# Optimization experiments

Hardware: AMD Instinct MI355X
Metric: run time of the kernel (lower is better)

Reference implementation:

```python
import jax, jax.numpy as jnp
import numpy as np

B, S, D = 4, 4096, 1024
GROUP = 256
HEAD = 128
INNER = 2048


def setup_inputs() -> dict:
    key = jax.random.key(0)
    ks = jax.random.split(key, 16)
    s = 0.02
    return {
        'x': jax.random.normal(ks[0], (B, S, D), jnp.float32),
        'Wv': jax.random.normal(ks[1], (D, INNER), jnp.float32) * s,
        'bv': jnp.zeros((INNER,), jnp.float32),
        'Wg': jax.random.normal(ks[2], (D, INNER), jnp.float32) * s,
        'bg': jnp.zeros((INNER,), jnp.float32),
        'Win': jax.random.normal(ks[3], (D, HEAD), jnp.float32) * s,
        'bin_': jnp.zeros((HEAD,), jnp.float32),
        'Wout': jax.random.normal(ks[4], (INNER, D), jnp.float32) * s,
        'bout': jnp.zeros((D,), jnp.float32),
        'g_qq': 1.0 + jax.random.normal(ks[5], (HEAD,), jnp.float32) * s,
        'b_qq': jnp.zeros((HEAD,), jnp.float32),
        'g_qk': 1.0 + jax.random.normal(ks[6], (HEAD,), jnp.float32) * s,
        'b_qk': jnp.zeros((HEAD,), jnp.float32),
        'g_lq': 1.0 + jax.random.normal(ks[7], (HEAD,), jnp.float32) * s,
        'b_lq': jnp.zeros((HEAD,), jnp.float32),
        'g_lk': 1.0 + jax.random.normal(ks[8], (HEAD,), jnp.float32) * s,
        'b_lk': jnp.zeros((HEAD,), jnp.float32),
    }


def reference(x, Wv, bv, Wg, bg, Win, bin_, Wout, bout,
              g_qq, b_qq, g_qk, b_qk, g_lq, b_lq, g_lk, b_lk):
    b, s, d = x.shape
    g = s // GROUP
    xc = x.reshape(b, g, GROUP, d)                       # [B,G,C,D]
    v = jax.nn.silu(xc @ Wv + bv)                        # [B,G,C,E]
    gate = jax.nn.silu(xc @ Wg + bg)                     # [B,G,C,E]
    x_ = jax.nn.silu(xc @ Win + bin_)                    # [B,G,C,H]
    quad_q = x_ * g_qq + b_qq
    quad_k = x_ * g_qk + b_qk
    lin_q = x_ * g_lq + b_lq
    lin_k = x_ * g_lk + b_lk
    # local quadratic relu^2 attention per chunk
    scale = jnp.asarray(INNER ** 0.5, x.dtype)           # v.size(-1)**0.5
    attn = jnp.einsum('bgns,bgms->bgnm', quad_q, quad_k) / scale
    causal_mask = jnp.triu(jnp.ones((GROUP, GROUP), bool), 1)
    attn = jnp.where(causal_mask, 0.0, attn)
    attn = jnp.square(jax.nn.relu(attn))
    v_quad = jnp.einsum('bgnm,bgme->bgne', attn, v)
    # global causal linear attention: exclusive cumsum of per-chunk k^T v over chunks
    kv = jnp.einsum('bgcs,bgce->bgse', lin_k, v)         # [B,G,H,E]
    kv = jnp.cumsum(kv, axis=1) - kv                     # exclusive over chunk dim
    v_lin = jnp.einsum('bgcs,bgse->bgce', lin_q, kv)
    o = (v_quad + v_lin) * gate
    o = o @ Wout + bout
    return o.reshape(b, s, d)
```

## Files before the change

### kernel.cpp

```cpp
#include <hip/hip_runtime.h>

typedef __attribute__((ext_vector_type(8))) short short8;
typedef __attribute__((ext_vector_type(4))) float floatx4;
typedef __attribute__((ext_vector_type(4))) unsigned short ushort4v;
typedef unsigned short u16;

#define DEV __device__ __forceinline__

DEV u16 f2bf(float f) {
  unsigned int u = __float_as_uint(f);
  u += 0x7fffu + ((u >> 16) & 1u);
  return (u16)(u >> 16);
}
DEV float bf2f(u16 h) { return __uint_as_float(((unsigned int)h) << 16); }
DEV float silu_f(float x) { return x / (1.f + __expf(-x)); }
DEV floatx4 fzero() { floatx4 z = {0.f, 0.f, 0.f, 0.f}; return z; }
DEV floatx4 mfma16(short8 a, short8 b, floatx4 c) {
  return __builtin_amdgcn_mfma_f32_16x16x32_bf16(a, b, c, 0, 0, 0);
}
DEV void gll16(const void* g, void* l) {
  __builtin_amdgcn_global_load_lds((__attribute__((address_space(1))) void*)g,
                                   (__attribute__((address_space(3))) void*)l,
                                   16, 0, 0);
}

__global__ __launch_bounds__(256) void cast_x_kernel(const float* __restrict__ x,
                                                     u16* __restrict__ xb, int n4) {
  int i = blockIdx.x * 256 + threadIdx.x;
  if (i >= n4) return;
  float4 v = ((const float4*)x)[i];
  ushort4v o;
  o[0] = f2bf(v.x); o[1] = f2bf(v.y); o[2] = f2bf(v.z); o[3] = f2bf(v.w);
  *(ushort4v*)&xb[(size_t)i * 4] = o;
}

__global__ __launch_bounds__(256) void transpose_cast_kernel(const float* __restrict__ W,
                                                             u16* __restrict__ WT,
                                                             int K, int N) {
  __shared__ u16 tile[32][36];
  int n0 = blockIdx.x * 32, k0 = blockIdx.y * 32;
  int t = threadIdx.x;
  int r = t >> 3, cs = (t & 7) * 4;
  float4 v = *(const float4*)&W[(size_t)(k0 + r) * N + n0 + cs];
  tile[r][cs + 0] = f2bf(v.x);
  tile[r][cs + 1] = f2bf(v.y);
  tile[r][cs + 2] = f2bf(v.z);
  tile[r][cs + 3] = f2bf(v.w);
  __syncthreads();
  ushort4v o;
  o[0] = tile[cs + 0][r];
  o[1] = tile[cs + 1][r];
  o[2] = tile[cs + 2][r];
  o[3] = tile[cs + 3][r];
  *(ushort4v*)&WT[(size_t)(n0 + r) * K + k0 + cs] = o;
}

DEV void wave_transposed_store(u16* __restrict__ Ct, long chunk_stride,
                               const u16* trw, int chunk, int cbase, int nbase,
                               int lane) {
#pragma unroll
  for (int it = 0; it < 8; ++it) {
    int e_l = it * 8 + (lane >> 3);
    int c_off = (lane & 7) * 8;
    short8 val = *(const short8*)&trw[e_l * 72 + c_off];
    *(short8*)&Ct[(size_t)chunk * chunk_stride + (size_t)(nbase + e_l) * 256 + cbase +
                  c_off] = val;
  }
}

__global__ __launch_bounds__(256, 2) void gemm_vg(
    const u16* __restrict__ A, const u16* __restrict__ Bv, const u16* __restrict__ Bg,
    const float* __restrict__ bvb, const float* __restrict__ bgb,
    u16* __restrict__ vT, u16* __restrict__ gate) {
  constexpr int K = 1024, N = 2048;
  __shared__ union {
    struct { u16 a[128 * 64]; u16 b[2][128 * 64]; } st;
    u16 tr[4 * 64 * 72];
  } sm;
  const int t = threadIdx.x;
  const int wave = t >> 6, lane = t & 63;
  const int l15 = lane & 15, l16 = lane >> 4;
  const int ell = blockIdx.x;
  const int xcd = ell & 7, i = ell >> 3;
  const int m0 = (xcd * 16 + (i >> 4)) * 128;
  const int n0 = (i & 15) * 128;
  const int wm = (wave >> 1) * 64, wn = (wave & 1) * 64;

  floatx4 accv[4][4], accg[4][4];
#pragma unroll
  for (int a = 0; a < 4; ++a)
#pragma unroll
    for (int b = 0; b < 4; ++b) { accv[a][b] = fzero(); accg[a][b] = fzero(); }

  const u16 *pa[4], *pbv[4], *pbg[4];
#pragma unroll
  for (int j = 0; j < 4; ++j) {
    const int c = t + 256 * j;
    const int r = c >> 3, p = c & 7;
    const int g = p ^ (r & 7);
    const size_t off = (size_t)r * K + g * 8;
    pa[j] = A + (size_t)m0 * K + off;
    pbv[j] = Bv + (size_t)n0 * K + off;
    pbg[j] = Bg + (size_t)n0 * K + off;
  }

  for (int k0 = 0; k0 < K; k0 += 64) {
    __syncthreads();
#pragma unroll
    for (int j = 0; j < 4; ++j) {
      const int d = (t + 256 * j) * 8;
      gll16(pa[j] + k0, &sm.st.a[d]);
      gll16(pbv[j] + k0, &sm.st.b[0][d]);
      gll16(pbg[j] + k0, &sm.st.b[1][d]);
    }
    __syncthreads();
#pragma unroll
    for (int s = 0; s < 2; ++s) {
      short8 af[4], b0[4], b1[4];
#pragma unroll
      for (int mi = 0; mi < 4; ++mi) {
        const int wr = wm + mi * 16 + l15;
        af[mi] = *(const short8*)&sm.st.a[wr * 64 + ((s * 4 + l16) ^ (wr & 7)) * 8];
      }
#pragma unroll
      for (int ni = 0; ni < 4; ++ni) {
        const int wr = wn + ni * 16 + l15;
        const int sl = wr * 64 + ((s * 4 + l16) ^ (wr & 7)) * 8;
        b0[ni] = *(const short8*)&sm.st.b[0][sl];
        b1[ni] = *(const short8*)&sm.st.b[1][sl];
      }
#pragma unroll
      for (int mi = 0; mi < 4; ++mi)
#pragma unroll
        for (int ni = 0; ni < 4; ++ni) {
          accv[mi][ni] = mfma16(af[mi], b0[ni], accv[mi][ni]);
          accg[mi][ni] = mfma16(af[mi], b1[ni], accg[mi][ni]);
        }
    }
  }
  __syncthreads();

  u16* trw = &sm.tr[wave * 64 * 72];
#pragma unroll
  for (int mi = 0; mi < 4; ++mi)
#pragma unroll
    for (int ni = 0; ni < 4; ++ni) {
      const float bc = bvb[n0 + wn + ni * 16 + l15];
      ushort4v p;
#pragma unroll
      for (int r = 0; r < 4; ++r) p[r] = f2bf(silu_f(accv[mi][ni][r] + bc));
      *(ushort4v*)&trw[(ni * 16 + l15) * 72 + mi * 16 + l16 * 4] = p;
    }
  wave_transposed_store(vT, 2048L * 256, trw, (m0 + wm) >> 8, (m0 + wm) & 255,
                        n0 + wn, lane);
#pragma unroll
  for (int mi = 0; mi < 4; ++mi)
#pragma unroll
    for (int ni = 0; ni < 4; ++ni) {
      const float bc = bgb[n0 + wn + ni * 16 + l15];
#pragma unroll
      for (int r = 0; r < 4; ++r)
        trw[(mi * 16 + l16 * 4 + r) * 72 + ni * 16 + l15] =
            f2bf(silu_f(accg[mi][ni][r] + bc));
    }
#pragma unroll
  for (int it = 0; it < 8; ++it) {
    const int m_l = it * 8 + (lane >> 3);
    const int n_off = (lane & 7) * 8;
    *(short8*)&gate[(size_t)(m0 + wm + m_l) * N + n0 + wn + n_off] =
        *(const short8*)&trw[m_l * 72 + n_off];
  }
}

template <int MODE>
__global__ __launch_bounds__(256) void gemm_bt(
    const u16* __restrict__ A, const u16* __restrict__ Bt, int M, int N, int K,
    int nshift, const float* __restrict__ bias, u16* __restrict__ Cn,
    float* __restrict__ Cf, u16* __restrict__ Ct, long ct_stride,
    u16* __restrict__ Cn2, u16* __restrict__ Cn3,
    const float* __restrict__ gqq, const float* __restrict__ bqq,
    const float* __restrict__ gqk, const float* __restrict__ bqk,
    const float* __restrict__ glq, const float* __restrict__ blq,
    const float* __restrict__ glk, const float* __restrict__ blk) {
  __shared__ union {
    struct { u16 a[128 * 64]; u16 b[128 * 64]; } st;
    u16 tr[4 * 64 * 72];
  } sm;
  const int t = threadIdx.x;
  const int wave = t >> 6, lane = t & 63;
  const int l15 = lane & 15, l16 = lane >> 4;
  const int ell = blockIdx.x;
  const int xcd = ell & 7, i = ell >> 3;
  const int mtiles_per_xcd = M >> 10;
  const int m0 = (xcd * mtiles_per_xcd + (i >> nshift)) * 128;
  const int n0 = (i & ((1 << nshift) - 1)) * 128;
  const int wm = (wave >> 1) * 64, wn = (wave & 1) * 64;

  floatx4 acc[4][4];
#pragma unroll
  for (int i2 = 0; i2 < 4; ++i2)
#pragma unroll
    for (int j = 0; j < 4; ++j) acc[i2][j] = fzero();

  const u16* pa[4];
  const u16* pb[4];
#pragma unroll
  for (int j = 0; j < 4; ++j) {
    const int c = t + 256 * j;
    const int r = c >> 3, p = c & 7;
    const int g = p ^ (r & 7);
    pa[j] = A + (size_t)(m0 + r) * K + g * 8;
    pb[j] = Bt + (size_t)(n0 + r) * K + g * 8;
  }

  for (int k0 = 0; k0 < K; k0 += 64) {
    __syncthreads();
#pragma unroll
    for (int j = 0; j < 4; ++j) {
      gll16(pa[j] + k0, &sm.st.a[(t + 256 * j) * 8]);
      gll16(pb[j] + k0, &sm.st.b[(t + 256 * j) * 8]);
    }
    __syncthreads();
#pragma unroll
    for (int s = 0; s < 2; ++s) {
      short8 af[4], bfr[4];
#pragma unroll
      for (int mi = 0; mi < 4; ++mi) {
        const int wr = wm + mi * 16 + l15;
        af[mi] = *(const short8*)&sm.st.a[wr * 64 + ((s * 4 + l16) ^ (wr & 7)) * 8];
      }
#pragma unroll
      for (int ni = 0; ni < 4; ++ni) {
        const int wr = wn + ni * 16 + l15;
        bfr[ni] = *(const short8*)&sm.st.b[wr * 64 + ((s * 4 + l16) ^ (wr & 7)) * 8];
      }
#pragma unroll
      for (int mi = 0; mi < 4; ++mi)
#pragma unroll
        for (int ni = 0; ni < 4; ++ni)
          acc[mi][ni] = mfma16(af[mi], bfr[ni], acc[mi][ni]);
    }
  }
  __syncthreads();

  if constexpr (MODE == 3) {
#pragma unroll
    for (int mi = 0; mi < 4; ++mi)
#pragma unroll
      for (int ni = 0; ni < 4; ++ni) {
        const int col = n0 + wn + ni * 16 + l15;
        const float bc = bias[col];
        const int row = m0 + wm + mi * 16 + l16 * 4;
#pragma unroll
        for (int r = 0; r < 4; ++r)
          Cf[(size_t)(row + r) * N + col] = acc[mi][ni][r] + bc;
      }
  } else {
    u16* trw = &sm.tr[wave * 64 * 72];
#pragma unroll
    for (int mi = 0; mi < 4; ++mi)
#pragma unroll
      for (int ni = 0; ni < 4; ++ni) {
        const int col = wn + ni * 16 + l15;
        const float bc = bias[col];
        const float Gqq = gqq[col], Bqq = bqq[col];
        const float Gqk = gqk[col], Bqk = bqk[col];
        const float Glq = glq[col], Blq = blq[col];
        const float Glk = glk[col], Blk = blk[col];
        const int row = m0 + wm + mi * 16 + l16 * 4;
        ushort4v p;
#pragma unroll
        for (int r = 0; r < 4; ++r) {
          const float sv = silu_f(acc[mi][ni][r] + bc);
          const size_t ad = (size_t)(row + r) * N + col;
          Cn[ad] = f2bf(sv * Gqq + Bqq);
          Cn2[ad] = f2bf(sv * Gqk + Bqk);
          Cn3[ad] = f2bf(sv * Glq + Blq);
          p[r] = f2bf(sv * Glk + Blk);
        }
        *(ushort4v*)&trw[(ni * 16 + l15) * 72 + mi * 16 + l16 * 4] = p;
      }
    wave_transposed_store(Ct, ct_stride, trw, (m0 + wm) >> 8, (m0 + wm) & 255, wn,
                          lane);
  }
}

__global__ __launch_bounds__(256) void kv_kernel(const u16* __restrict__ vT,
                                                 const u16* __restrict__ lkT,
                                                 u16* __restrict__ kv) {
  const int chunk = blockIdx.y;
  const int et = blockIdx.x;
  const int w = threadIdx.x >> 6, lane = threadIdx.x & 63;
  const int l15 = lane & 15, l16 = lane >> 4;
  const size_t vb = (size_t)chunk * (2048 * 256) + (size_t)et * (128 * 256);
  const size_t lb = (size_t)chunk * (128 * 256);
  const int we = (w >> 1) * 64, wh = (w & 1) * 64;
  floatx4 acc[4][4];
#pragma unroll
  for (int i = 0; i < 4; ++i)
#pragma unroll
    for (int j = 0; j < 4; ++j) acc[i][j] = fzero();
  for (int kk = 0; kk < 8; ++kk) {
    short8 av[4], bv[4];
#pragma unroll
    for (int mi = 0; mi < 4; ++mi)
      av[mi] = *(const short8*)&vT[vb + (size_t)(we + mi * 16 + l15) * 256 + kk * 32 +
                                   l16 * 8];
#pragma unroll
    for (int ni = 0; ni < 4; ++ni)
      bv[ni] = *(const short8*)&lkT[lb + (size_t)(wh + ni * 16 + l15) * 256 + kk * 32 +
                                    l16 * 8];
#pragma unroll
    for (int mi = 0; mi < 4; ++mi)
#pragma unroll
      for (int ni = 0; ni < 4; ++ni) acc[mi][ni] = mfma16(av[mi], bv[ni], acc[mi][ni]);
  }
  u16* out = kv + (size_t)chunk * (2048 * 128);
#pragma unroll
  for (int mi = 0; mi < 4; ++mi)
#pragma unroll
    for (int ni = 0; ni < 4; ++ni) {
      const int h = wh + ni * 16 + l15;
      const int e = et * 128 + we + mi * 16 + l16 * 4;
#pragma unroll
      for (int r = 0; r < 4; ++r) out[(size_t)(e + r) * 128 + h] = f2bf(acc[mi][ni][r]);
    }
}

__global__ __launch_bounds__(256) void cumsum_kernel(u16* __restrict__ kv) {
  const int idx = blockIdx.x * 256 + threadIdx.x;
  const int b = blockIdx.y;
  float s = 0.f;
  for (int g = 0; g < 16; ++g) {
    const size_t a = (size_t)(b * 16 + g) * 262144 + idx;
    const float v = bf2f(kv[a]);
    kv[a] = f2bf(s);
    s += v;
  }
}

__global__ __launch_bounds__(256) void attn_kernel(
    const u16* __restrict__ qq, const u16* __restrict__ qk, const u16* __restrict__ lq,
    const u16* __restrict__ vT, const u16* __restrict__ kvT,
    u16* __restrict__ gate_op) {
  __shared__ u16 S[64][264];
  const int chunk = blockIdx.y;
  const int e0 = blockIdx.x * 256;
  const int tok0 = chunk * 256;
  const int w = threadIdx.x >> 6, lane = threadIdx.x & 63;
  const int l15 = lane & 15, l16 = lane >> 4;
  const float isc = 0.022097086912079608f;
  const size_t vbase = (size_t)chunk * (2048 * 256);
  const size_t kbase = (size_t)chunk * (2048 * 128);
  const int ew = e0 + w * 64;

  for (int ns = 0; ns < 4; ++ns) {
    const int r0 = ns * 64 + w * 16;
    short8 af[4];
#pragma unroll
    for (int kk = 0; kk < 4; ++kk)
      af[kk] = *(const short8*)&qq[(size_t)(tok0 + r0 + l15) * 128 + kk * 32 + l16 * 8];
    const int mt_cnt = (r0 >> 4) + 1;
    const int mt_all = (ns + 1) * 4;
    const int srow = w * 16 + l16 * 4;
    for (int mt = 0; mt < mt_all; ++mt) {
      if (mt < mt_cnt) {
        floatx4 a = fzero();
#pragma unroll
        for (int kk = 0; kk < 4; ++kk) {
          short8 bq =
              *(const short8*)&qk[(size_t)(tok0 + mt * 16 + l15) * 128 + kk * 32 +
                                  l16 * 8];
          a = mfma16(af[kk], bq, a);
        }
        const int mcol = mt * 16 + l15;
#pragma unroll
        for (int r = 0; r < 4; ++r) {
          const int nrow = r0 + l16 * 4 + r;
          float sv = a[r] * isc;
          sv = (mcol <= nrow) ? sv : 0.f;
          sv = fmaxf(sv, 0.f);
          S[srow + r][mcol] = f2bf(sv * sv);
        }
      } else {
#pragma unroll
        for (int r = 0; r < 4; ++r) S[srow + r][mt * 16 + l15] = (u16)0;
      }
    }
    __syncthreads();

    floatx4 acc[4][4];
#pragma unroll
    for (int i = 0; i < 4; ++i)
#pragma unroll
      for (int j = 0; j < 4; ++j) acc[i][j] = fzero();

    const int ks = (ns + 1) * 2;
    for (int kk = 0; kk < ks; ++kk) {
      short8 sa[4];
#pragma unroll
      for (int nt = 0; nt < 4; ++nt)
        sa[nt] = *(const short8*)&S[nt * 16 + l15][kk * 32 + l16 * 8];
#pragma unroll
      for (int ei = 0; ei < 4; ++ei) {
        short8 vb = *(const short8*)&vT[vbase + (size_t)(ew + ei * 16 + l15) * 256 +
                                        kk * 32 + l16 * 8];
#pragma unroll
        for (int nt = 0; nt < 4; ++nt) acc[nt][ei] = mfma16(sa[nt], vb, acc[nt][ei]);
      }
    }
#pragma unroll
    for (int kk = 0; kk < 4; ++kk) {
      short8 la[4];
#pragma unroll
      for (int nt = 0; nt < 4; ++nt)
        la[nt] = *(const short8*)&lq[(size_t)(tok0 + ns * 64 + nt * 16 + l15) * 128 +
                                     kk * 32 + l16 * 8];
#pragma unroll
      for (int ei = 0; ei < 4; ++ei) {
        short8 kb = *(const short8*)&kvT[kbase + (size_t)(ew + ei * 16 + l15) * 128 +
                                         kk * 32 + l16 * 8];
#pragma unroll
        for (int nt = 0; nt < 4; ++nt) acc[nt][ei] = mfma16(la[nt], kb, acc[nt][ei]);
      }
    }
#pragma unroll
    for (int nt = 0; nt < 4; ++nt)
#pragma unroll
      for (int ei = 0; ei < 4; ++ei) {
        const int e_g = ew + ei * 16 + l15;
        const int nb = tok0 + ns * 64 + nt * 16 + l16 * 4;
#pragma unroll
        for (int r = 0; r < 4; ++r) {
          const size_t ad = (size_t)(nb + r) * 2048 + e_g;
          const float gv = bf2f(gate_op[ad]);
          gate_op[ad] = f2bf(acc[nt][ei][r] * gv);
        }
      }
    __syncthreads();
  }
}

extern "C" void kernel_launch(void* const* d_in, const int* in_sizes, int n_in,
                              void* d_out, int out_size, void* d_ws, size_t ws_size,
                              hipStream_t stream) {
  (void)in_sizes; (void)n_in; (void)out_size; (void)ws_size;
  const float* x = (const float*)d_in[0];
  const float* Wv = (const float*)d_in[1];
  const float* bv = (const float*)d_in[2];
  const float* Wg = (const float*)d_in[3];
  const float* bg = (const float*)d_in[4];
  const float* Win = (const float*)d_in[5];
  const float* bin = (const float*)d_in[6];
  const float* Wout = (const float*)d_in[7];
  const float* bout = (const float*)d_in[8];
  const float* gqq = (const float*)d_in[9];
  const float* bqq = (const float*)d_in[10];
  const float* gqk = (const float*)d_in[11];
  const float* bqk = (const float*)d_in[12];
  const float* glq = (const float*)d_in[13];
  const float* blq = (const float*)d_in[14];
  const float* glk = (const float*)d_in[15];
  const float* blk = (const float*)d_in[16];

  char* p = (char*)d_ws;
  u16* xb = (u16*)p;   p += (size_t)16384 * 1024 * 2;
  u16* wvT = (u16*)p;  p += (size_t)2048 * 1024 * 2;
  u16* wgT = (u16*)p;  p += (size_t)2048 * 1024 * 2;
  u16* winT = (u16*)p; p += (size_t)128 * 1024 * 2;
  u16* woT = (u16*)p;  p += (size_t)1024 * 2048 * 2;
  u16* vTb = (u16*)p;  p += (size_t)64 * 2048 * 256 * 2;
  u16* gate = (u16*)p; p += (size_t)16384 * 2048 * 2;
  u16* qqb = (u16*)p;  p += (size_t)16384 * 128 * 2;
  u16* qkb = (u16*)p;  p += (size_t)16384 * 128 * 2;
  u16* lqb = (u16*)p;  p += (size_t)16384 * 128 * 2;
  u16* lkTb = (u16*)p; p += (size_t)64 * 128 * 256 * 2;
  u16* kvb = (u16*)p;  p += (size_t)64 * 2048 * 128 * 2;

  cast_x_kernel<<<16384, 256, 0, stream>>>(x, xb, 4194304);
  transpose_cast_kernel<<<dim3(64, 32), 256, 0, stream>>>(Wv, wvT, 1024, 2048);
  transpose_cast_kernel<<<dim3(64, 32), 256, 0, stream>>>(Wg, wgT, 1024, 2048);
  transpose_cast_kernel<<<dim3(4, 32), 256, 0, stream>>>(Win, winT, 1024, 128);
  transpose_cast_kernel<<<dim3(32, 64), 256, 0, stream>>>(Wout, woT, 2048, 1024);

  gemm_vg<<<2048, 256, 0, stream>>>(xb, wvT, wgT, bv, bg, vTb, gate);
  gemm_bt<2><<<128, 256, 0, stream>>>(
      xb, winT, 16384, 128, 1024, 0, bin, qqb, nullptr, lkTb, 128L * 256, qkb, lqb,
      gqq, bqq, gqk, bqk, glq, blq, glk, blk);

  kv_kernel<<<dim3(16, 64), 256, 0, stream>>>(vTb, lkTb, kvb);
  cumsum_kernel<<<dim3(1024, 4), 256, 0, stream>>>(kvb);
  attn_kernel<<<dim3(8, 64), 256, 0, stream>>>(qqb, qkb, lqb, vTb, kvb, gate);

  gemm_bt<3><<<1024, 256, 0, stream>>>(
      gate, woT, 16384, 1024, 2048, 3, bout, nullptr, (float*)d_out, nullptr, 0,
      nullptr, nullptr, nullptr, nullptr, nullptr, nullptr, nullptr, nullptr, nullptr,
      nullptr);
}
```

Before: 560.0 us.

## Replace projection GEMMs with 256x256 eight-wave multi-stage pipelined GEMM kernel

```diff
diff --git a/kernel.cpp b/kernel.cpp
--- a/kernel.cpp
+++ b/kernel.cpp
@@ -68,107 +68,167 @@
   }
 }
 
-__global__ __launch_bounds__(256, 2) void gemm_vg(
-    const u16* __restrict__ A, const u16* __restrict__ Bv, const u16* __restrict__ Bg,
-    const float* __restrict__ bvb, const float* __restrict__ bgb,
-    u16* __restrict__ vT, u16* __restrict__ gate) {
-  constexpr int K = 1024, N = 2048;
-  __shared__ union {
-    struct { u16 a[128 * 64]; u16 b[2][128 * 64]; } st;
-    u16 tr[4 * 64 * 72];
-  } sm;
+
+#define PH(SA, SB, NIA, NIB, VML, RDA, STG, HH)                                \
+  {                                                                            \
+    asm volatile("s_waitcnt vmcnt(" #VML ")" ::: "memory");                    \
+    if (RDA) {                                                                 \
+      _Pragma("unroll") for (int mi_ = 0; mi_ < 8; ++mi_)                      \
+          af[mi_] = *(const short8*)&lds[((SA) * 1024 + aoff + mi_ * 64) * 8]; \
+    }                                                                          \
+    bf0 = *(const short8*)&lds[((SB) * 1024 + boff + (NIA) * 64) * 8];         \
+    bf1 = *(const short8*)&lds[((SB) * 1024 + boff + (NIB) * 64) * 8];         \
+    if (STG) STAGE(HH);                                                        \
+    asm volatile("" ::: "memory");                                             \
+    __builtin_amdgcn_s_barrier();                                              \
+    asm volatile("" ::: "memory");                                             \
+    __builtin_amdgcn_s_setprio(1);                                             \
+    _Pragma("unroll") for (int mi_ = 0; mi_ < 8; ++mi_) {                      \
+      acc[mi_][NIA] = mfma16(af[mi_], bf0, acc[mi_][NIA]);                     \
+      acc[mi_][NIB] = mfma16(af[mi_], bf1, acc[mi_][NIB]);                     \
+    }                                                                          \
+    __builtin_amdgcn_s_setprio(0);                                             \
+    asm volatile("" ::: "memory");                                             \
+    __builtin_amdgcn_s_barrier();                                              \
+    asm volatile("" ::: "memory");                                             \
+  }
+
+template <int MODE>
+__global__ __launch_bounds__(512, 2) void gemm8(
+    const u16* __restrict__ A, const u16* __restrict__ Bt,
+    const float* __restrict__ bias0, const float* __restrict__ bias1,
+    u16* __restrict__ vT, u16* __restrict__ gate, float* __restrict__ Cf) {
+  constexpr int KK = (MODE == 0) ? 1024 : 2048;
+  constexpr int NN = (MODE == 0) ? 4096 : 1024;
+  constexpr int NT = KK / 64;
+  constexpr int NSH = (MODE == 0) ? 4 : 2;
+
+  __shared__ u16 lds[8 * 8192];
+
   const int t = threadIdx.x;
   const int wave = t >> 6, lane = t & 63;
   const int l15 = lane & 15, l16 = lane >> 4;
-  const int ell = blockIdx.x;
-  const int xcd = ell & 7, i = ell >> 3;
-  const int m0 = (xcd * 16 + (i >> 4)) * 128;
-  const int n0 = (i & 15) * 128;
-  const int wm = (wave >> 1) * 64, wn = (wave & 1) * 64;
-
-  floatx4 accv[4][4], accg[4][4];
-#pragma unroll
-  for (int a = 0; a < 4; ++a)
-#pragma unroll
-    for (int b = 0; b < 4; ++b) { accv[a][b] = fzero(); accg[a][b] = fzero(); }
-
-  const u16 *pa[4], *pbv[4], *pbg[4];
-#pragma unroll
-  for (int j = 0; j < 4; ++j) {
-    const int c = t + 256 * j;
-    const int r = c >> 3, p = c & 7;
-    const int g = p ^ (r & 7);
-    const size_t off = (size_t)r * K + g * 8;
-    pa[j] = A + (size_t)m0 * K + off;
-    pbv[j] = Bv + (size_t)n0 * K + off;
-    pbg[j] = Bg + (size_t)n0 * K + off;
-  }
-
-  for (int k0 = 0; k0 < K; k0 += 64) {
-    __syncthreads();
-#pragma unroll
-    for (int j = 0; j < 4; ++j) {
-      const int d = (t + 256 * j) * 8;
-      gll16(pa[j] + k0, &sm.st.a[d]);
-      gll16(pbv[j] + k0, &sm.st.b[0][d]);
-      gll16(pbg[j] + k0, &sm.st.b[1][d]);
-    }
-    __syncthreads();
-#pragma unroll
-    for (int s = 0; s < 2; ++s) {
-      short8 af[4], b0[4], b1[4];
-#pragma unroll
-      for (int mi = 0; mi < 4; ++mi) {
-        const int wr = wm + mi * 16 + l15;
-        af[mi] = *(const short8*)&sm.st.a[wr * 64 + ((s * 4 + l16) ^ (wr & 7)) * 8];
-      }
+  const int b = blockIdx.x;
+  const int xcd = b & 7, i = b >> 3;
+  const int m0 = (xcd * 8 + (i >> NSH)) * 256;
+  const int n0 = (i & ((1 << NSH) - 1)) * 256;
+  const int wm = wave >> 2, wn = wave & 3;
+
+  const int o0 = wave * 128 + lane;
+  const int r0 = o0 >> 2;
+  const int p0 = (o0 & 3) ^ ((r0 >> 1) & 3);
+  const u16* srcA = A + (size_t)(m0 + r0) * KK + p0 * 8;
+  const u16* srcB = Bt + (size_t)(n0 + r0) * KK + p0 * 8;
+
+  auto STAGE = [&](int h) {
+    const int slot = h & 7;
+    const int koff = (h >> 2) * 64 + ((h >> 1) & 1) * 32;
+    u16* dst = &lds[slot * 8192 + o0 * 8];
+    const u16* s = ((h & 1) ? srcB : srcA) + koff;
+    gll16(s, dst);
+    gll16(s + 16 * KK, dst + 512);
+  };
+
+  const int rA = wm * 128 + l15;
+  const int aoff = rA * 4 + (l16 ^ ((rA >> 1) & 3));
+  const int rB = wn * 64 + l15;
+  const int boff = rB * 4 + (l16 ^ ((rB >> 1) & 3));
+
+  floatx4 acc[8][4];
+#pragma unroll
+  for (int a = 0; a < 8; ++a)
+#pragma unroll
+    for (int c = 0; c < 4; ++c) acc[a][c] = fzero();
+  short8 af[8], bf0, bf1;
+
+#pragma unroll
+  for (int h = 0; h < 7; ++h) STAGE(h);
+  asm volatile("s_waitcnt vmcnt(10)" ::: "memory");
+  asm volatile("" ::: "memory");
+  __builtin_amdgcn_s_barrier();
+  asm volatile("" ::: "memory");
+
+  for (int T = 0; T < NT - 2; ++T) {
+    const int s0 = (T & 1) * 4;
+    PH(s0, s0 + 1, 0, 1, 8, 1, 1, 4 * T + 7)
+    PH(s0, s0 + 1, 2, 3, 8, 0, 1, 4 * T + 8)
+    PH(s0 + 2, s0 + 3, 0, 1, 8, 1, 1, 4 * T + 9)
+    PH(s0 + 2, s0 + 3, 2, 3, 8, 0, 1, 4 * T + 10)
+  }
+  {
+    const int s0 = ((NT - 2) & 1) * 4;
+    PH(s0, s0 + 1, 0, 1, 8, 1, 1, 4 * (NT - 2) + 7)
+    PH(s0, s0 + 1, 2, 3, 8, 0, 0, 0)
+    PH(s0 + 2, s0 + 3, 0, 1, 6, 1, 0, 0)
+    PH(s0 + 2, s0 + 3, 2, 3, 4, 0, 0, 0)
+  }
+  {
+    const int s0 = ((NT - 1) & 1) * 4;
+    PH(s0, s0 + 1, 0, 1, 2, 1, 0, 0)
+    PH(s0, s0 + 1, 2, 3, 0, 0, 0, 0)
+    PH(s0 + 2, s0 + 3, 0, 1, 0, 1, 0, 0)
+    PH(s0 + 2, s0 + 3, 2, 3, 0, 0, 0, 0)
+  }
+
+  if constexpr (MODE == 0) {
+    const int chunk = m0 >> 8;
+    u16* trw = &lds[wave * (64 * 72)];
+    if (n0 < 2048) {
+      const int e0 = n0 + wn * 64;
+#pragma unroll
+      for (int th = 0; th < 2; ++th) {
+#pragma unroll
+        for (int mi2 = 0; mi2 < 4; ++mi2) {
+          const int mi = th * 4 + mi2;
+#pragma unroll
+          for (int ni = 0; ni < 4; ++ni) {
+            const float bc = bias0[e0 + ni * 16 + l15];
+            ushort4v pk;
+#pragma unroll
+            for (int r = 0; r < 4; ++r) pk[r] = f2bf(silu_f(acc[mi][ni][r] + bc));
+            *(ushort4v*)&trw[(ni * 16 + l15) * 72 + mi2 * 16 + l16 * 4] = pk;
+          }
+        }
+        wave_transposed_store(vT, 2048L * 256, trw, chunk, wm * 128 + th * 64, e0,
+                              lane);
+      }
+    } else {
+      const int c0 = n0 - 2048 + wn * 64;
+#pragma unroll
+      for (int th = 0; th < 2; ++th) {
+#pragma unroll
+        for (int mi2 = 0; mi2 < 4; ++mi2) {
+          const int mi = th * 4 + mi2;
+#pragma unroll
+          for (int ni = 0; ni < 4; ++ni) {
+            const float bc = bias1[c0 + ni * 16 + l15];
+#pragma unroll
+            for (int r = 0; r < 4; ++r)
+              trw[(mi2 * 16 + l16 * 4 + r) * 72 + ni * 16 + l15] =
+                  f2bf(silu_f(acc[mi][ni][r] + bc));
+          }
+        }
+#pragma unroll
+        for (int it = 0; it < 8; ++it) {
+          const int m_l = it * 8 + (lane >> 3);
+          const int n_off = (lane & 7) * 8;
+          *(short8*)&gate[(size_t)(m0 + wm * 128 + th * 64 + m_l) * 2048 + c0 +
+                          n_off] = *(const short8*)&trw[m_l * 72 + n_off];
+        }
+      }
+    }
+  } else {
+#pragma unroll
+    for (int mi = 0; mi < 8; ++mi)
 #pragma unroll
       for (int ni = 0; ni < 4; ++ni) {
-        const int wr = wn + ni * 16 + l15;
-        const int sl = wr * 64 + ((s * 4 + l16) ^ (wr & 7)) * 8;
-        b0[ni] = *(const short8*)&sm.st.b[0][sl];
-        b1[ni] = *(const short8*)&sm.st.b[1][sl];
-      }
-#pragma unroll
-      for (int mi = 0; mi < 4; ++mi)
-#pragma unroll
-        for (int ni = 0; ni < 4; ++ni) {
-          accv[mi][ni] = mfma16(af[mi], b0[ni], accv[mi][ni]);
-          accg[mi][ni] = mfma16(af[mi], b1[ni], accg[mi][ni]);
-        }
-    }
-  }
-  __syncthreads();
-
-  u16* trw = &sm.tr[wave * 64 * 72];
-#pragma unroll
-  for (int mi = 0; mi < 4; ++mi)
-#pragma unroll
-    for (int ni = 0; ni < 4; ++ni) {
-      const float bc = bvb[n0 + wn + ni * 16 + l15];
-      ushort4v p;
-#pragma unroll
-      for (int r = 0; r < 4; ++r) p[r] = f2bf(silu_f(accv[mi][ni][r] + bc));
-      *(ushort4v*)&trw[(ni * 16 + l15) * 72 + mi * 16 + l16 * 4] = p;
-    }
-  wave_transposed_store(vT, 2048L * 256, trw, (m0 + wm) >> 8, (m0 + wm) & 255,
-                        n0 + wn, lane);
-#pragma unroll
-  for (int mi = 0; mi < 4; ++mi)
-#pragma unroll
-    for (int ni = 0; ni < 4; ++ni) {
-      const float bc = bgb[n0 + wn + ni * 16 + l15];
-#pragma unroll
-      for (int r = 0; r < 4; ++r)
-        trw[(mi * 16 + l16 * 4 + r) * 72 + ni * 16 + l15] =
-            f2bf(silu_f(accg[mi][ni][r] + bc));
-    }
-#pragma unroll
-  for (int it = 0; it < 8; ++it) {
-    const int m_l = it * 8 + (lane >> 3);
-    const int n_off = (lane & 7) * 8;
-    *(short8*)&gate[(size_t)(m0 + wm + m_l) * N + n0 + wn + n_off] =
-        *(const short8*)&trw[m_l * 72 + n_off];
+        const int col = n0 + wn * 64 + ni * 16 + l15;
+        const float bc = bias0[col];
+        const int row = m0 + wm * 128 + mi * 16 + l16 * 4;
+#pragma unroll
+        for (int r = 0; r < 4; ++r)
+          Cf[(size_t)(row + r) * NN + col] = acc[mi][ni][r] + bc;
+      }
   }
 }
 
@@ -483,7 +543,8 @@
   transpose_cast_kernel<<<dim3(4, 32), 256, 0, stream>>>(Win, winT, 1024, 128);
   transpose_cast_kernel<<<dim3(32, 64), 256, 0, stream>>>(Wout, woT, 2048, 1024);
 
-  gemm_vg<<<2048, 256, 0, stream>>>(xb, wvT, wgT, bv, bg, vTb, gate);
+  gemm8<0><<<1024, 512, 0, stream>>>(xb, wvT, bv, bg, vTb, gate, nullptr);
+
   gemm_bt<2><<<128, 256, 0, stream>>>(
       xb, winT, 16384, 128, 1024, 0, bin, qqb, nullptr, lkTb, 128L * 256, qkb, lqb,
       gqq, bqq, gqk, bqk, glq, blq, glk, blk);
@@ -492,8 +553,6 @@
   cumsum_kernel<<<dim3(1024, 4), 256, 0, stream>>>(kvb);
   attn_kernel<<<dim3(8, 64), 256, 0, stream>>>(qqb, qkb, lqb, vTb, kvb, gate);
 
-  gemm_bt<3><<<1024, 256, 0, stream>>>(
-      gate, woT, 16384, 1024, 2048, 3, bout, nullptr, (float*)d_out, nullptr, 0,
-      nullptr, nullptr, nullptr, nullptr, nullptr, nullptr, nullptr, nullptr, nullptr,
-      nullptr);
-}
+  gemm8<1><<<256, 512, 0, stream>>>(gate, woT, bout, nullptr, nullptr, nullptr,
+                                    (float*)d_out);
+}
```

After: 567.0 us. Within noise of the previous version (+1.2%).

## Precompute relu-squared attention scores once per chunk in a separate kernel

Applied to the files above, without the earlier changes.

```diff
diff --git a/kernel.cpp b/kernel.cpp
--- a/kernel.cpp
+++ b/kernel.cpp
@@ -339,56 +339,64 @@
   }
 }
 
-__global__ __launch_bounds__(256) void attn_kernel(
-    const u16* __restrict__ qq, const u16* __restrict__ qk, const u16* __restrict__ lq,
+__global__ __launch_bounds__(256) void s_kernel(const u16* __restrict__ qq,
+                                                const u16* __restrict__ qk,
+                                                u16* __restrict__ Sg) {
+  const int chunk = blockIdx.x >> 2;
+  const int ns = blockIdx.x & 3;
+  const int tok0 = chunk * 256;
+  const int w = threadIdx.x >> 6, lane = threadIdx.x & 63;
+  const int l15 = lane & 15, l16 = lane >> 4;
+  const float isc = 0.022097086912079608f;
+  const int r0 = ns * 64 + w * 16;
+  short8 af[4];
+#pragma unroll
+  for (int kk = 0; kk < 4; ++kk)
+    af[kk] = *(const short8*)&qq[(size_t)(tok0 + r0 + l15) * 128 + kk * 32 + l16 * 8];
+  const int mt_cnt = (r0 >> 4) + 1;
+  const int mt_all = (ns + 1) * 4;
+  u16* sc = Sg + (size_t)chunk * 65536;
+  const int srow = r0 + l16 * 4;
+  for (int mt = 0; mt < mt_all; ++mt) {
+    if (mt < mt_cnt) {
+      floatx4 a = fzero();
+#pragma unroll
+      for (int kk = 0; kk < 4; ++kk) {
+        short8 bq = *(const short8*)&qk[(size_t)(tok0 + mt * 16 + l15) * 128 +
+                                        kk * 32 + l16 * 8];
+        a = mfma16(af[kk], bq, a);
+      }
+      const int mcol = mt * 16 + l15;
+#pragma unroll
+      for (int r = 0; r < 4; ++r) {
+        const int nrow = r0 + l16 * 4 + r;
+        float sv = a[r] * isc;
+        sv = (mcol <= nrow) ? sv : 0.f;
+        sv = fmaxf(sv, 0.f);
+        sc[(size_t)(srow + r) * 256 + mcol] = f2bf(sv * sv);
+      }
+    } else {
+#pragma unroll
+      for (int r = 0; r < 4; ++r) sc[(size_t)(srow + r) * 256 + mt * 16 + l15] = (u16)0;
+    }
+  }
+}
+
+__global__ __launch_bounds__(256) void attn2_kernel(
+    const u16* __restrict__ Sg, const u16* __restrict__ lq,
     const u16* __restrict__ vT, const u16* __restrict__ kvT,
     u16* __restrict__ gate_op) {
-  __shared__ u16 S[64][264];
   const int chunk = blockIdx.y;
   const int e0 = blockIdx.x * 256;
   const int tok0 = chunk * 256;
   const int w = threadIdx.x >> 6, lane = threadIdx.x & 63;
   const int l15 = lane & 15, l16 = lane >> 4;
-  const float isc = 0.022097086912079608f;
   const size_t vbase = (size_t)chunk * (2048 * 256);
   const size_t kbase = (size_t)chunk * (2048 * 128);
+  const u16* sc = Sg + (size_t)chunk * 65536;
   const int ew = e0 + w * 64;
 
   for (int ns = 0; ns < 4; ++ns) {
-    const int r0 = ns * 64 + w * 16;
-    short8 af[4];
-#pragma unroll
-    for (int kk = 0; kk < 4; ++kk)
-      af[kk] = *(const short8*)&qq[(size_t)(tok0 + r0 + l15) * 128 + kk * 32 + l16 * 8];
-    const int mt_cnt = (r0 >> 4) + 1;
-    const int mt_all = (ns + 1) * 4;
-    const int srow = w * 16 + l16 * 4;
-    for (int mt = 0; mt < mt_all; ++mt) {
-      if (mt < mt_cnt) {
-        floatx4 a = fzero();
-#pragma unroll
-        for (int kk = 0; kk < 4; ++kk) {
-          short8 bq =
-              *(const short8*)&qk[(size_t)(tok0 + mt * 16 + l15) * 128 + kk * 32 +
-                                  l16 * 8];
-          a = mfma16(af[kk], bq, a);
-        }
-        const int mcol = mt * 16 + l15;
-#pragma unroll
-        for (int r = 0; r < 4; ++r) {
-          const int nrow = r0 + l16 * 4 + r;
-          float sv = a[r] * isc;
-          sv = (mcol <= nrow) ? sv : 0.f;
-          sv = fmaxf(sv, 0.f);
-          S[srow + r][mcol] = f2bf(sv * sv);
-        }
-      } else {
-#pragma unroll
-        for (int r = 0; r < 4; ++r) S[srow + r][mt * 16 + l15] = (u16)0;
-      }
-    }
-    __syncthreads();
-
     floatx4 acc[4][4];
 #pragma unroll
     for (int i = 0; i < 4; ++i)
@@ -400,7 +408,8 @@
       short8 sa[4];
 #pragma unroll
       for (int nt = 0; nt < 4; ++nt)
-        sa[nt] = *(const short8*)&S[nt * 16 + l15][kk * 32 + l16 * 8];
+        sa[nt] = *(const short8*)&sc[(size_t)(ns * 64 + nt * 16 + l15) * 256 +
+                                     kk * 32 + l16 * 8];
 #pragma unroll
       for (int ei = 0; ei < 4; ++ei) {
         short8 vb = *(const short8*)&vT[vbase + (size_t)(ew + ei * 16 + l15) * 256 +
@@ -437,7 +446,6 @@
           gate_op[ad] = f2bf(acc[nt][ei][r] * gv);
         }
       }
-    __syncthreads();
   }
 }
 
@@ -476,6 +484,7 @@
   u16* lqb = (u16*)p;  p += (size_t)16384 * 128 * 2;
   u16* lkTb = (u16*)p; p += (size_t)64 * 128 * 256 * 2;
   u16* kvb = (u16*)p;  p += (size_t)64 * 2048 * 128 * 2;
+  u16* Sgb = (u16*)p;  p += (size_t)64 * 256 * 256 * 2;
 
   cast_x_kernel<<<16384, 256, 0, stream>>>(x, xb, 4194304);
   transpose_cast_kernel<<<dim3(64, 32), 256, 0, stream>>>(Wv, wvT, 1024, 2048);
@@ -488,9 +497,10 @@
       xb, winT, 16384, 128, 1024, 0, bin, qqb, nullptr, lkTb, 128L * 256, qkb, lqb,
       gqq, bqq, gqk, bqk, glq, blq, glk, blk);
 
+  s_kernel<<<256, 256, 0, stream>>>(qqb, qkb, Sgb);
   kv_kernel<<<dim3(16, 64), 256, 0, stream>>>(vTb, lkTb, kvb);
   cumsum_kernel<<<dim3(1024, 4), 256, 0, stream>>>(kvb);
-  attn_kernel<<<dim3(8, 64), 256, 0, stream>>>(qqb, qkb, lqb, vTb, kvb, gate);
+  attn2_kernel<<<dim3(8, 64), 256, 0, stream>>>(Sgb, lqb, vTb, kvb, gate);
 
   gemm_bt<3><<<1024, 256, 0, stream>>>(
       gate, woT, 16384, 1024, 2048, 3, bout, nullptr, (float*)d_out, nullptr, 0,
```

Result: slower. 637.7 us (+13.9%).
